# Kernel optimization log

Measured on AMD Instinct MI355X. Metric: run time of the kernel, lower is better.

## Reference

```python
import jax, jax.numpy as jnp
import numpy as np

B, C, H, W = 8, 384, 32, 32
NH = 6
HD = C // NH          # 64
T = H * W             # 1024
EPS = 1e-5            # torch InstanceNorm2d default


def setup_inputs() -> dict:
    key = jax.random.key(0)
    ks = jax.random.split(key, 8)
    s = 1.0 / np.sqrt(C)  # keep pre-softmax logits in a sane range
    x = jax.random.normal(ks[0], (B, C, H, W), dtype=jnp.float32)
    Wq = jax.random.normal(ks[1], (C, C), dtype=jnp.float32) * s
    Wk = jax.random.normal(ks[2], (C, C), dtype=jnp.float32) * s
    Wv = jax.random.normal(ks[3], (C, C), dtype=jnp.float32) * s
    head_w = jax.random.normal(ks[4], (NH, NH), dtype=jnp.float32) * (1.0 / np.sqrt(NH))
    gamma = jnp.ones((NH,), dtype=jnp.float32)
    beta = jnp.zeros((NH,), dtype=jnp.float32)
    projW = jax.random.normal(ks[5], (C, C), dtype=jnp.float32) * s
    projb = jnp.zeros((C,), dtype=jnp.float32)
    return {"x": x, "Wq": Wq, "Wk": Wk, "Wv": Wv, "head_w": head_w,
            "gamma": gamma, "beta": beta, "projW": projW, "projb": projb}


def reference(x, Wq, Wk, Wv, head_w, gamma, beta, projW, projb):
    b, c, h, w = x.shape
    t = h * w
    scale = HD ** (-0.5)
    xf = x.reshape(b, c, t)                               # [B,C,T]
    # 1x1 convs == channel GEMMs; conv weight [Cout,Cin]
    q = jnp.einsum('oc,bct->bot', Wq, xf).reshape(b, NH, HD, t)
    k = jnp.einsum('oc,bct->bot', Wk, xf).reshape(b, NH, HD, t)
    v = jnp.einsum('oc,bct->bot', Wv, xf).reshape(b, NH, HD, t)
    # raw scores [B,h,T,T], scaled
    scores = jnp.einsum('bhdq,bhdt->bhqt', q, k) * scale
    # cross-head 1x1 conv mix: out-head g from in-head h
    mixed = jnp.einsum('gh,bhqt->bgqt', head_w, scores)
    attn = jax.nn.softmax(mixed, axis=-1)
    # InstanceNorm2d over spatial dims (q,T) per (b,head), biased variance
    mean = jnp.mean(attn, axis=(2, 3), keepdims=True)
    var = jnp.var(attn, axis=(2, 3), keepdims=True)
    attn = (attn - mean) * jax.lax.rsqrt(var + EPS)
    attn = attn * gamma[None, :, None, None] + beta[None, :, None, None]
    # value matmul: v is [B,h,d,T]
    out = jnp.einsum('bhqt,bhdt->bhqd', attn, v)          # [B,h,T,d]
    # faithful row-major reshape (matches torch .view(B, T, C))
    out = out.reshape(b, t, c)
    y = out @ projW.T + projb                              # Linear(C,C)
    return jnp.transpose(y, (0, 2, 1)).reshape(b, c, h, w)
```

## Files before the change

kernel.cpp:

```cpp
#include <hip/hip_runtime.h>
#include <hip/hip_bf16.h>
#include <cstdint>

typedef __bf16 bf16_t;
typedef __bf16 bf16x8 __attribute__((ext_vector_type(8)));
typedef float  f32x4  __attribute__((ext_vector_type(4)));

#define MFMA16(a, b, c) __builtin_amdgcn_mfma_f32_16x16x32_bf16((a), (b), (c), 0, 0, 0)

constexpr int BB = 8, CC = 384, NHH = 6, TT = 1024;

union U8 { uint4 u; bf16_t h[8]; };
union U2 { unsigned int u; bf16_t h[2]; };

struct CastArgs {
    const void* src[9];
    bf16_t*     dst[9];
    int         n[9];
};

__global__ __launch_bounds__(256) void cast_kernel(CastArgs a)
{
    const bool isbf = (((const unsigned short*)a.src[5])[0] == 0x3F80u);
    const int ai = blockIdx.y;
    const int n  = a.n[ai];
    bf16_t* dst  = a.dst[ai];
    const int t0     = (blockIdx.x * 256 + threadIdx.x) * 8;
    const int stride = gridDim.x * 256 * 8;
    if (isbf) {
        const bf16_t* s = (const bf16_t*)a.src[ai];
        for (int idx = t0; idx < n; idx += stride) {
            if (idx + 8 <= n) *(uint4*)(dst + idx) = *(const uint4*)(s + idx);
            else for (int j = 0; idx + j < n; ++j) dst[idx + j] = s[idx + j];
        }
    } else {
        const float* s = (const float*)a.src[ai];
        for (int idx = t0; idx < n; idx += stride) {
            if (idx + 8 <= n) {
                f32x4 v0 = *(const f32x4*)(s + idx);
                f32x4 v1 = *(const f32x4*)(s + idx + 4);
                U8 o;
                #pragma unroll
                for (int j = 0; j < 4; ++j) { o.h[j] = (bf16_t)v0[j]; o.h[4 + j] = (bf16_t)v1[j]; }
                *(uint4*)(dst + idx) = o.u;
            } else for (int j = 0; idx + j < n; ++j) dst[idx + j] = (bf16_t)s[idx + j];
        }
    }
}

__global__ __launch_bounds__(256) void qkv_kernel(
    const bf16_t* __restrict__ x,
    const bf16_t* __restrict__ Wq,
    const bf16_t* __restrict__ Wk,
    const bf16_t* __restrict__ Wv,
    bf16_t* __restrict__ qT,
    bf16_t* __restrict__ kT,
    bf16_t* __restrict__ vm)
{
    const int og = blockIdx.x;
    const int tt = blockIdx.y;
    const int b  = blockIdx.z;
    const int t0 = tt * 64;
    const int tid  = threadIdx.x;
    const int lane = tid & 63;
    const int wid  = tid >> 6;
    const int quad = lane >> 4;
    const int l16  = lane & 15;

    __shared__ __align__(16) bf16_t xT[64][CC + 8];

    {
        const bf16_t* xb = x + (size_t)b * CC * TT;
        const int tq = tid & 7;
        const int cp = tid >> 3;
        #pragma unroll
        for (int pass = 0; pass < 6; ++pass) {
            const int c = (pass * 32 + cp) * 2;
            U8 r0, r1;
            r0.u = *(const uint4*)(xb + (size_t)c * TT + t0 + tq * 8);
            r1.u = *(const uint4*)(xb + (size_t)(c + 1) * TT + t0 + tq * 8);
            #pragma unroll
            for (int j = 0; j < 8; ++j) {
                U2 p; p.h[0] = r0.h[j]; p.h[1] = r1.h[j];
                *(unsigned int*)&xT[tq * 8 + j][c] = p.u;
            }
        }
    }
    __syncthreads();

    const bf16_t* W = (og < 2) ? Wq : (og < 4) ? Wk : Wv;
    const int obase = (og & 1) * 192 + wid * 48;

    if (og < 4) {
        f32x4 acc[3][4];
        const f32x4 zero = {0.f, 0.f, 0.f, 0.f};
        #pragma unroll
        for (int mi = 0; mi < 3; ++mi)
            #pragma unroll
            for (int ni = 0; ni < 4; ++ni) acc[mi][ni] = zero;

        for (int k0 = 0; k0 < CC; k0 += 32) {
            bf16x8 afr[3];
            #pragma unroll
            for (int mi = 0; mi < 3; ++mi)
                afr[mi] = *(const bf16x8*)(W + (size_t)(obase + mi * 16 + l16) * CC + k0 + quad * 8);
            #pragma unroll
            for (int ni = 0; ni < 4; ++ni) {
                bf16x8 bfr = *(const bf16x8*)&xT[ni * 16 + l16][k0 + quad * 8];
                #pragma unroll
                for (int mi = 0; mi < 3; ++mi)
                    acc[mi][ni] = MFMA16(afr[mi], bfr, acc[mi][ni]);
            }
        }

        bf16_t* dst = (og < 2) ? qT : kT;
        #pragma unroll
        for (int mi = 0; mi < 3; ++mi)
            #pragma unroll
            for (int ni = 0; ni < 4; ++ni) {
                const int o0 = obase + mi * 16 + quad * 4;
                const int tl = t0 + ni * 16 + l16;
                U2 lo2, hi2;
                lo2.h[0] = (bf16_t)acc[mi][ni][0]; lo2.h[1] = (bf16_t)acc[mi][ni][1];
                hi2.h[0] = (bf16_t)acc[mi][ni][2]; hi2.h[1] = (bf16_t)acc[mi][ni][3];
                uint2 pk; pk.x = lo2.u; pk.y = hi2.u;
                *(uint2*)(dst + ((size_t)b * TT + tl) * CC + o0) = pk;
            }
    } else {
        f32x4 acc[4][3];
        const f32x4 zero = {0.f, 0.f, 0.f, 0.f};
        #pragma unroll
        for (int mi = 0; mi < 4; ++mi)
            #pragma unroll
            for (int ni = 0; ni < 3; ++ni) acc[mi][ni] = zero;

        for (int k0 = 0; k0 < CC; k0 += 32) {
            bf16x8 bfr[3];
            #pragma unroll
            for (int ni = 0; ni < 3; ++ni)
                bfr[ni] = *(const bf16x8*)(W + (size_t)(obase + ni * 16 + l16) * CC + k0 + quad * 8);
            #pragma unroll
            for (int mi = 0; mi < 4; ++mi) {
                bf16x8 afr = *(const bf16x8*)&xT[mi * 16 + l16][k0 + quad * 8];
                #pragma unroll
                for (int ni = 0; ni < 3; ++ni)
                    acc[mi][ni] = MFMA16(afr, bfr[ni], acc[mi][ni]);
            }
        }

        #pragma unroll
        for (int mi = 0; mi < 4; ++mi)
            #pragma unroll
            for (int ni = 0; ni < 3; ++ni) {
                const int ol  = obase + ni * 16 + l16;
                const int tl0 = mi * 16 + quad * 4;
                U2 lo2, hi2;
                lo2.h[0] = (bf16_t)acc[mi][ni][0]; lo2.h[1] = (bf16_t)acc[mi][ni][1];
                hi2.h[0] = (bf16_t)acc[mi][ni][2]; hi2.h[1] = (bf16_t)acc[mi][ni][3];
                uint2 pk; pk.x = lo2.u; pk.y = hi2.u;
                *(uint2*)(vm + ((size_t)b * CC + ol) * TT + t0 + tl0) = pk;
            }
    }
}

__global__ __launch_bounds__(256) void vrow_kernel(const bf16_t* __restrict__ vm,
                                                   float* __restrict__ vrs)
{
    const int bg = blockIdx.x;
    const int d  = threadIdx.x & 63;
    const int qr = threadIdx.x >> 6;
    const bf16_t* row = vm + ((size_t)(bg / 6) * CC + (bg % 6) * 64 + d) * TT + qr * 256;
    float s = 0.f;
    for (int i = 0; i < 256; i += 8) {
        U8 v; v.u = *(const uint4*)(row + i);
        #pragma unroll
        for (int j = 0; j < 8; ++j) s += (float)v.h[j];
    }
    __shared__ float red[4][64];
    red[qr][d] = s;
    __syncthreads();
    if (qr == 0) vrs[bg * 64 + d] = red[0][d] + red[1][d] + red[2][d] + red[3][d];
}

__global__ __launch_bounds__(512, 2) void fused_attn(
    const bf16_t* __restrict__ qT,
    const bf16_t* __restrict__ kT,
    const bf16_t* __restrict__ vm,
    const bf16_t* __restrict__ head_w,
    float* __restrict__ Up,
    float* __restrict__ lp,
    float* __restrict__ l2p)
{
    const int L  = blockIdx.x;
    const int b  = L & 7;
    const int rr = L >> 3;
    const int qt = rr & 15;
    const int th = rr >> 4;

    const int tid = threadIdx.x, lane = tid & 63, wid = tid >> 6;
    const int quad = lane >> 4, l16 = lane & 15;

    __shared__ __align__(16) bf16_t sm[49152];
    bf16_t* Ks = sm;
    bf16_t* Ps = sm + 12288;
    bf16_t* Vs = sm + 24576;
    __shared__ float smix[36];

    if (tid < 36) smix[tid] = 0.125f * (float)head_w[tid];

    const int T0 = th * 512;

    const int tsub = wid & 1;
    const int sqh  = wid >> 1;
    const int pqg  = wid >> 1;
    const int pgg  = wid & 1;

    bf16x8 qf[6][2];
    {
        const bf16_t* Qb = qT + ((size_t)b * TT + qt * 64 + sqh * 16 + l16) * CC + quad * 8;
        #pragma unroll
        for (int kk = 0; kk < 6; ++kk)
            #pragma unroll
            for (int k2 = 0; k2 < 2; ++k2)
                qf[kk][k2] = *(const bf16x8*)(Qb + kk * 64 + k2 * 32);
    }

    const bf16_t* ksrc[3]; const bf16_t* vsrc[3];
    int kdst[3], vdst[3];
    #pragma unroll
    for (int it = 0; it < 3; ++it) {
        const int f  = it * 512 + tid;
        const int kk = f >> 8, krow = (f >> 3) & 31, kch = f & 7;
        ksrc[it] = kT + ((size_t)b * TT + T0 + krow) * CC + kk * 64 + (kch ^ (krow & 7)) * 8;
        kdst[it] = f * 8;
        const int vrow = f >> 2, vch = f & 3;
        vsrc[it] = vm + ((size_t)b * CC + vrow) * TT + T0 + (vch ^ ((vrow >> 1) & 3)) * 8;
        vdst[it] = f * 8;
    }

    uint4 kreg[3], vreg[3];
    #pragma unroll
    for (int it = 0; it < 3; ++it) {
        kreg[it] = *(const uint4*)ksrc[it];
        vreg[it] = *(const uint4*)vsrc[it];
    }
    __syncthreads();

    float mixc[36];
    #pragma unroll
    for (int j = 0; j < 36; ++j)
        mixc[j] = __uint_as_float(__builtin_amdgcn_readfirstlane(__float_as_uint(smix[j])));

    #pragma unroll
    for (int it = 0; it < 3; ++it) {
        *(uint4*)&Ks[kdst[it]] = kreg[it];
        *(uint4*)&Vs[vdst[it]] = vreg[it];
        kreg[it] = *(const uint4*)(ksrc[it] + 32 * CC);
        vreg[it] = *(const uint4*)(vsrc[it] + 32);
    }
    __syncthreads();

    f32x4 Uacc[3][4];
    const f32x4 zero = {0.f, 0.f, 0.f, 0.f};
    #pragma unroll
    for (int hh = 0; hh < 3; ++hh)
        #pragma unroll
        for (int n2 = 0; n2 < 4; ++n2) Uacc[hh][n2] = zero;
    float lacc[6]  = {0.f, 0.f, 0.f, 0.f, 0.f, 0.f};
    float l2acc[6] = {0.f, 0.f, 0.f, 0.f, 0.f, 0.f};

    const int arow  = (tsub * 16 + l16) * 64;
    const int aswz0 = ((quad)     ^ (l16 & 7)) * 8;
    const int aswz1 = ((4 + quad) ^ (l16 & 7)) * 8;
    const int prow  = (sqh * 16 + l16) * 32;
    const int pswzW = ((tsub * 2 + (quad >> 1)) ^ ((l16 >> 1) & 3)) * 8 + (quad & 1) * 4;
    const int parow = (pqg * 16 + l16) * 32;
    const int pswzR = (quad ^ ((l16 >> 1) & 3)) * 8;

    for (int t = 0; t < 16; ++t) {
        f32x4 S[6];
        #pragma unroll
        for (int kk = 0; kk < 6; ++kk) {
            bf16x8 a0 = *(const bf16x8*)&Ks[kk * 2048 + arow + aswz0];
            bf16x8 a1 = *(const bf16x8*)&Ks[kk * 2048 + arow + aswz1];
            S[kk] = MFMA16(a0, qf[kk][0], zero);
            S[kk] = MFMA16(a1, qf[kk][1], S[kk]);
        }
        uint2 pk[6];
        #pragma unroll
        for (int g = 0; g < 6; ++g) {
            float mp[4];
            #pragma unroll
            for (int r = 0; r < 4; ++r) {
                float m = mixc[g * 6] * S[0][r];
                #pragma unroll
                for (int h = 1; h < 6; ++h) m += mixc[g * 6 + h] * S[h][r];
                const float p = __expf(fminf(m, 60.0f));
                lacc[g]  += p;
                l2acc[g] += p * p;
                mp[r] = p;
            }
            U2 lo, hi;
            lo.h[0] = (bf16_t)mp[0]; lo.h[1] = (bf16_t)mp[1];
            hi.h[0] = (bf16_t)mp[2]; hi.h[1] = (bf16_t)mp[3];
            pk[g].x = lo.u; pk[g].y = hi.u;
        }
        __syncthreads();
        #pragma unroll
        for (int it = 0; it < 3; ++it) {
            *(uint4*)&Ks[kdst[it]] = kreg[it];
            *(uint4*)&Vs[((t + 1) & 1) * 12288 + vdst[it]] = vreg[it];
        }
        #pragma unroll
        for (int g = 0; g < 6; ++g)
            *(uint2*)&Ps[g * 2048 + prow + pswzW] = pk[g];
        {
            const int nt = ((t + 2) & 15) * 32;
            #pragma unroll
            for (int it = 0; it < 3; ++it) {
                kreg[it] = *(const uint4*)(ksrc[it] + nt * CC);
                vreg[it] = *(const uint4*)(vsrc[it] + nt);
            }
        }
        __syncthreads();
        const int vb = (t & 1) * 12288;
        #pragma unroll
        for (int hh = 0; hh < 3; ++hh) {
            const int g = pgg * 3 + hh;
            bf16x8 ap = *(const bf16x8*)&Ps[g * 2048 + parow + pswzR];
            #pragma unroll
            for (int n2 = 0; n2 < 4; ++n2) {
                bf16x8 bv = *(const bf16x8*)&Vs[vb + (g * 64 + n2 * 16 + l16) * 32 + pswzR];
                Uacc[hh][n2] = MFMA16(ap, bv, Uacc[hh][n2]);
            }
        }
        __syncthreads();
    }

    float* lredL  = (float*)sm;
    float* l2redL = lredL + 768;
    #pragma unroll
    for (int g = 0; g < 6; ++g) {
        float l = lacc[g], l2 = l2acc[g];
        l  += __shfl_xor(l, 16, 64);  l  += __shfl_xor(l, 32, 64);
        l2 += __shfl_xor(l2, 16, 64); l2 += __shfl_xor(l2, 32, 64);
        if (quad == 0) {
            lredL [wid * 96 + g * 16 + l16] = l;
            l2redL[wid * 96 + g * 16 + l16] = l2;
        }
    }
    __syncthreads();
    if (tid < 384) {
        const int g = tid >> 6, q = tid & 63;
        const int w0 = (q >> 4) * 2, lo = q & 15;
        const float l  = lredL [w0 * 96 + g * 16 + lo] + lredL [(w0 + 1) * 96 + g * 16 + lo];
        const float l2 = l2redL[w0 * 96 + g * 16 + lo] + l2redL[(w0 + 1) * 96 + g * 16 + lo];
        const size_t o = ((size_t)th * 48 + b * 6 + g) * TT + qt * 64 + q;
        lp[o] = l; l2p[o] = l2;
    }

    #pragma unroll
    for (int hh = 0; hh < 3; ++hh) {
        const int g = pgg * 3 + hh;
        float* Ub = Up + ((((size_t)th * 8 + b) * 6 + g) * TT + qt * 64 + pqg * 16) * 64;
        #pragma unroll
        for (int n2 = 0; n2 < 4; ++n2)
            #pragma unroll
            for (int r = 0; r < 4; ++r)
                Ub[(size_t)(quad * 4 + r) * 64 + n2 * 16 + l16] = Uacc[hh][n2][r];
    }
}

__global__ __launch_bounds__(256) void stats_kernel(
    const float* __restrict__ lp, const float* __restrict__ l2p,
    float* __restrict__ linv, float* __restrict__ sq)
{
    const int bg = blockIdx.x, tid = threadIdx.x;
    float c = 0.f;
    for (int q = tid; q < TT; q += 256) {
        const float l  = lp [(size_t)bg * TT + q] + lp [(size_t)(48 + bg) * TT + q];
        const float l2 = l2p[(size_t)bg * TT + q] + l2p[(size_t)(48 + bg) * TT + q];
        const float inv = 1.0f / l;
        linv[bg * TT + q] = inv;
        c += l2 * inv * inv;
    }
    #pragma unroll
    for (int off = 1; off < 64; off <<= 1) c += __shfl_xor(c, off, 64);
    __shared__ float red[4];
    if ((tid & 63) == 0) red[tid >> 6] = c;
    __syncthreads();
    if (tid == 0) sq[bg] = red[0] + red[1] + red[2] + red[3];
}

__global__ __launch_bounds__(256) void proj_kernel(
    const float* __restrict__ Up,
    const float* __restrict__ linv,
    const float* __restrict__ vrs,
    const float* __restrict__ sumsq,
    const bf16_t* __restrict__ gamma,
    const bf16_t* __restrict__ beta,
    const bf16_t* __restrict__ projW,
    const bf16_t* __restrict__ projb,
    float* __restrict__ out)
{
    const int ts = blockIdx.x;
    const int b  = blockIdx.y;
    const int t0 = ts * 32;
    const int tid = threadIdx.x, lane = tid & 63, wid = tid >> 6;
    const int quad = lane >> 4, l16 = lane & 15;

    __shared__ float Ac[6], Cc[6], pb[CC];
    if (tid < 6) {
        const float ss  = sumsq[b * NHH + tid];
        const float var = fmaxf(ss - 1.0f, 0.0f) * (1.0f / 1048576.0f);
        const float a   = (float)gamma[tid] * rsqrtf(var + 1e-5f);
        Ac[tid] = a;
        Cc[tid] = (float)beta[tid] - a * (1.0f / 1024.0f);
    }
    for (int i = tid; i < CC; i += 256) pb[i] = (float)projb[i];
    __syncthreads();

    f32x4 acc[6][2];
    const f32x4 zero = {0.f, 0.f, 0.f, 0.f};
    #pragma unroll
    for (int mi = 0; mi < 6; ++mi)
        #pragma unroll
        for (int ni = 0; ni < 2; ++ni) acc[mi][ni] = zero;

    const float* U0 = Up + (size_t)b * (NHH * TT * 64);
    const float* U1 = Up + (size_t)(8 + b) * (NHH * TT * 64);
    for (int k0 = 0; k0 < CC; k0 += 32) {
        bf16x8 bfr[2];
        #pragma unroll
        for (int ni = 0; ni < 2; ++ni) {
            const int tl = t0 + ni * 16 + l16;
            const int baseoff = tl * CC + k0 + quad * 8;
            const int hh = baseoff >> 16;
            const float li = linv[b * 6144 + (baseoff >> 6)];
            const float A  = Ac[hh];
            const float Cb = Cc[hh];
            f32x4 a0 = *(const f32x4*)(U0 + baseoff);
            f32x4 a1 = *(const f32x4*)(U0 + baseoff + 4);
            f32x4 c0 = *(const f32x4*)(U1 + baseoff);
            f32x4 c1 = *(const f32x4*)(U1 + baseoff + 4);
            U8 z;
            #pragma unroll
            for (int j = 0; j < 8; ++j) {
                const int d = (baseoff + j) & 63;
                const float uv = ((j < 4) ? (a0[j] + c0[j]) : (a1[j - 4] + c1[j - 4])) * li;
                z.h[j] = (bf16_t)(A * uv + Cb * vrs[(b * NHH + hh) * 64 + d]);
            }
            bfr[ni] = *(const bf16x8*)&z;
        }
        #pragma unroll
        for (int mi = 0; mi < 6; ++mi) {
            const int o = wid * 96 + mi * 16 + l16;
            bf16x8 afr = *(const bf16x8*)(projW + (size_t)o * CC + k0 + quad * 8);
            #pragma unroll
            for (int ni = 0; ni < 2; ++ni)
                acc[mi][ni] = MFMA16(afr, bfr[ni], acc[mi][ni]);
        }
    }

    #pragma unroll
    for (int mi = 0; mi < 6; ++mi)
        #pragma unroll
        for (int ni = 0; ni < 2; ++ni)
            #pragma unroll
            for (int r = 0; r < 4; ++r) {
                const int o  = wid * 96 + mi * 16 + quad * 4 + r;
                const int tl = t0 + ni * 16 + l16;
                out[((size_t)b * CC + o) * TT + tl] = acc[mi][ni][r] + pb[o];
            }
}

extern "C" void kernel_launch(void* const* d_in, const int* in_sizes, int n_in,
                              void* d_out, int out_size, void* d_ws, size_t ws_size,
                              hipStream_t stream)
{
    float* outp = (float*)d_out;
    char* ws = (char*)d_ws;

    size_t off = 0;
    auto alloc = [&](size_t bytes) {
        void* p = ws + off;
        off += (bytes + 255) & ~(size_t)255;
        return p;
    };

    const size_t szT = (size_t)BB * TT * CC * sizeof(bf16_t);

    bf16_t* cx  = (bf16_t*)alloc(szT);
    bf16_t* cWq = (bf16_t*)alloc((size_t)CC * CC * 2);
    bf16_t* cWk = (bf16_t*)alloc((size_t)CC * CC * 2);
    bf16_t* cWv = (bf16_t*)alloc((size_t)CC * CC * 2);
    bf16_t* cPW = (bf16_t*)alloc((size_t)CC * CC * 2);
    bf16_t* chw = (bf16_t*)alloc(64 * 2);
    bf16_t* cg  = (bf16_t*)alloc(64 * 2);
    bf16_t* cb  = (bf16_t*)alloc(64 * 2);
    bf16_t* cpb = (bf16_t*)alloc(CC * 2);
    bf16_t* qTb = (bf16_t*)alloc(szT);
    bf16_t* kTb = (bf16_t*)alloc(szT);
    bf16_t* vmb = (bf16_t*)alloc(szT);
    float*  Uh  = (float*)alloc((size_t)2 * BB * NHH * TT * 64 * sizeof(float));
    float*  lpb = (float*)alloc((size_t)2 * 48 * TT * sizeof(float));
    float*  l2b = (float*)alloc((size_t)2 * 48 * TT * sizeof(float));
    float*  lv  = (float*)alloc((size_t)48 * TT * sizeof(float));
    float*  vr  = (float*)alloc(48 * 64 * sizeof(float));
    float*  sq  = (float*)alloc(48 * sizeof(float));

    CastArgs ca;
    bf16_t* dsts[9] = {cx, cWq, cWk, cWv, chw, cg, cb, cPW, cpb};
    for (int i = 0; i < 9; ++i) {
        ca.src[i] = d_in[i];
        ca.dst[i] = dsts[i];
        ca.n[i]   = in_sizes[i];
    }

    cast_kernel<<<dim3(192, 9), 256, 0, stream>>>(ca);
    qkv_kernel<<<dim3(6, 16, 8), 256, 0, stream>>>(cx, cWq, cWk, cWv, qTb, kTb, vmb);
    vrow_kernel<<<48, 256, 0, stream>>>(vmb, vr);
    fused_attn<<<256, 512, 0, stream>>>(qTb, kTb, vmb, chw, Uh, lpb, l2b);
    stats_kernel<<<48, 256, 0, stream>>>(lpb, l2b, lv, sq);
    proj_kernel<<<dim3(32, 8), 256, 0, stream>>>(Uh, lv, vr, sq, cg, cb, cPW, cpb, outp);
}
```

Baseline: 223.7 us.

## Fuse casts into consumers, fold V row sums, restructure attention pipeline

Removes the separate cast kernel, so qkv and proj read fp32 inputs and convert inline. The V row-sum kernel is folded into qkv through atomics. The attention kernel moves to 256-thread blocks with a 4-way key split, async global-to-LDS loads, and in-register P transposition via ds_bpermute instead of an LDS round-trip. This cuts launches and LDS traffic, but doubles the partial-U buffer that proj must read and sum, and adds more partial stats.

New measurement: 343.3 us. 1.53x slower.

```diff
diff --git a/kernel.cpp b/kernel.cpp
--- a/kernel.cpp
+++ b/kernel.cpp
@@ -5,6 +5,7 @@
 typedef __bf16 bf16_t;
 typedef __bf16 bf16x8 __attribute__((ext_vector_type(8)));
 typedef float  f32x4  __attribute__((ext_vector_type(4)));
+typedef int    i32x4  __attribute__((ext_vector_type(4)));
 
 #define MFMA16(a, b, c) __builtin_amdgcn_mfma_f32_16x16x32_bf16((a), (b), (c), 0, 0, 0)
 
@@ -12,50 +13,30 @@
 
 union U8 { uint4 u; bf16_t h[8]; };
 union U2 { unsigned int u; bf16_t h[2]; };
-
-struct CastArgs {
-    const void* src[9];
-    bf16_t*     dst[9];
-    int         n[9];
-};
-
-__global__ __launch_bounds__(256) void cast_kernel(CastArgs a)
-{
-    const bool isbf = (((const unsigned short*)a.src[5])[0] == 0x3F80u);
-    const int ai = blockIdx.y;
-    const int n  = a.n[ai];
-    bf16_t* dst  = a.dst[ai];
-    const int t0     = (blockIdx.x * 256 + threadIdx.x) * 8;
-    const int stride = gridDim.x * 256 * 8;
-    if (isbf) {
-        const bf16_t* s = (const bf16_t*)a.src[ai];
-        for (int idx = t0; idx < n; idx += stride) {
-            if (idx + 8 <= n) *(uint4*)(dst + idx) = *(const uint4*)(s + idx);
-            else for (int j = 0; idx + j < n; ++j) dst[idx + j] = s[idx + j];
-        }
-    } else {
-        const float* s = (const float*)a.src[ai];
-        for (int idx = t0; idx < n; idx += stride) {
-            if (idx + 8 <= n) {
-                f32x4 v0 = *(const f32x4*)(s + idx);
-                f32x4 v1 = *(const f32x4*)(s + idx + 4);
-                U8 o;
-                #pragma unroll
-                for (int j = 0; j < 4; ++j) { o.h[j] = (bf16_t)v0[j]; o.h[4 + j] = (bf16_t)v1[j]; }
-                *(uint4*)(dst + idx) = o.u;
-            } else for (int j = 0; idx + j < n; ++j) dst[idx + j] = (bf16_t)s[idx + j];
-        }
-    }
+union I4B { i32x4 i; bf16x8 v; };
+
+static __device__ __forceinline__ void gload_lds16(const void* g, void* l) {
+    __builtin_amdgcn_global_load_lds((const __attribute__((address_space(1))) void*)g,
+                                     (__attribute__((address_space(3))) void*)l, 16, 0, 0);
+}
+
+static __device__ __forceinline__ bf16x8 cvt8(const float* p) {
+    f32x4 a = *(const f32x4*)p, b = *(const f32x4*)(p + 4);
+    U8 o;
+    #pragma unroll
+    for (int j = 0; j < 4; ++j) { o.h[j] = (bf16_t)a[j]; o.h[4 + j] = (bf16_t)b[j]; }
+    return *(bf16x8*)&o;
 }
 
 __global__ __launch_bounds__(256) void qkv_kernel(
-    const bf16_t* __restrict__ x,
-    const bf16_t* __restrict__ Wq,
-    const bf16_t* __restrict__ Wk,
-    const bf16_t* __restrict__ Wv,
+    const float* __restrict__ x,
+    const float* __restrict__ Wq,
+    const float* __restrict__ Wk,
+    const float* __restrict__ Wv,
     bf16_t* __restrict__ qT,
     bf16_t* __restrict__ kT,
-    bf16_t* __restrict__ vm)
+    bf16_t* __restrict__ vm,
+    float*  __restrict__ vrs)
 {
     const int og = blockIdx.x;
     const int tt = blockIdx.y;
@@ -70,25 +51,28 @@
     __shared__ __align__(16) bf16_t xT[64][CC + 8];
 
     {
-        const bf16_t* xb = x + (size_t)b * CC * TT;
+        const float* xb = x + (size_t)b * CC * TT;
         const int tq = tid & 7;
         const int cp = tid >> 3;
         #pragma unroll
         for (int pass = 0; pass < 6; ++pass) {
             const int c = (pass * 32 + cp) * 2;
-            U8 r0, r1;
-            r0.u = *(const uint4*)(xb + (size_t)c * TT + t0 + tq * 8);
-            r1.u = *(const uint4*)(xb + (size_t)(c + 1) * TT + t0 + tq * 8);
+            const float* r0 = xb + (size_t)c * TT + t0 + tq * 8;
+            const float* r1 = r0 + TT;
+            f32x4 a0 = *(const f32x4*)r0, a1 = *(const f32x4*)(r0 + 4);
+            f32x4 b0 = *(const f32x4*)r1, b1 = *(const f32x4*)(r1 + 4);
             #pragma unroll
             for (int j = 0; j < 8; ++j) {
-                U2 p; p.h[0] = r0.h[j]; p.h[1] = r1.h[j];
+                U2 p;
+                p.h[0] = (bf16_t)((j < 4) ? a0[j] : a1[j - 4]);
+                p.h[1] = (bf16_t)((j < 4) ? b0[j] : b1[j - 4]);
                 *(unsigned int*)&xT[tq * 8 + j][c] = p.u;
             }
         }
     }
     __syncthreads();
 
-    const bf16_t* W = (og < 2) ? Wq : (og < 4) ? Wk : Wv;
+    const float* W = (og < 2) ? Wq : (og < 4) ? Wk : Wv;
     const int obase = (og & 1) * 192 + wid * 48;
 
     if (og < 4) {
@@ -103,7 +87,7 @@
             bf16x8 afr[3];
             #pragma unroll
             for (int mi = 0; mi < 3; ++mi)
-                afr[mi] = *(const bf16x8*)(W + (size_t)(obase + mi * 16 + l16) * CC + k0 + quad * 8);
+                afr[mi] = cvt8(W + (size_t)(obase + mi * 16 + l16) * CC + k0 + quad * 8);
             #pragma unroll
             for (int ni = 0; ni < 4; ++ni) {
                 bf16x8 bfr = *(const bf16x8*)&xT[ni * 16 + l16][k0 + quad * 8];
@@ -138,7 +122,7 @@
             bf16x8 bfr[3];
             #pragma unroll
             for (int ni = 0; ni < 3; ++ni)
-                bfr[ni] = *(const bf16x8*)(W + (size_t)(obase + ni * 16 + l16) * CC + k0 + quad * 8);
+                bfr[ni] = cvt8(W + (size_t)(obase + ni * 16 + l16) * CC + k0 + quad * 8);
             #pragma unroll
             for (int mi = 0; mi < 4; ++mi) {
                 bf16x8 afr = *(const bf16x8*)&xT[mi * 16 + l16][k0 + quad * 8];
@@ -160,33 +144,27 @@
                 uint2 pk; pk.x = lo2.u; pk.y = hi2.u;
                 *(uint2*)(vm + ((size_t)b * CC + ol) * TT + t0 + tl0) = pk;
             }
-    }
-}
-
-__global__ __launch_bounds__(256) void vrow_kernel(const bf16_t* __restrict__ vm,
-                                                   float* __restrict__ vrs)
-{
-    const int bg = blockIdx.x;
-    const int d  = threadIdx.x & 63;
-    const int qr = threadIdx.x >> 6;
-    const bf16_t* row = vm + ((size_t)(bg / 6) * CC + (bg % 6) * 64 + d) * TT + qr * 256;
-    float s = 0.f;
-    for (int i = 0; i < 256; i += 8) {
-        U8 v; v.u = *(const uint4*)(row + i);
-        #pragma unroll
-        for (int j = 0; j < 8; ++j) s += (float)v.h[j];
-    }
-    __shared__ float red[4][64];
-    red[qr][d] = s;
-    __syncthreads();
-    if (qr == 0) vrs[bg * 64 + d] = red[0][d] + red[1][d] + red[2][d] + red[3][d];
-}
-
-__global__ __launch_bounds__(512, 2) void fused_attn(
+
+        #pragma unroll
+        for (int ni = 0; ni < 3; ++ni) {
+            float s = 0.f;
+            #pragma unroll
+            for (int mi = 0; mi < 4; ++mi)
+                #pragma unroll
+                for (int r = 0; r < 4; ++r) s += acc[mi][ni][r];
+            s += __shfl_xor(s, 16, 64);
+            s += __shfl_xor(s, 32, 64);
+            if (quad == 0)
+                atomicAdd(&vrs[b * CC + obase + ni * 16 + l16], s);
+        }
+    }
+}
+
+__global__ __launch_bounds__(256, 2) void fused_attn(
     const bf16_t* __restrict__ qT,
     const bf16_t* __restrict__ kT,
     const bf16_t* __restrict__ vm,
-    const bf16_t* __restrict__ head_w,
+    const float*  __restrict__ head_w,
     float* __restrict__ Up,
     float* __restrict__ lp,
     float* __restrict__ l2p)
@@ -196,178 +174,162 @@
     const int rr = L >> 3;
     const int qt = rr & 15;
     const int th = rr >> 4;
+    const int T0 = th * 256;
 
     const int tid = threadIdx.x, lane = tid & 63, wid = tid >> 6;
     const int quad = lane >> 4, l16 = lane & 15;
 
-    __shared__ __align__(16) bf16_t sm[49152];
+    __shared__ __align__(16) bf16_t sm[36864];
     bf16_t* Ks = sm;
-    bf16_t* Ps = sm + 12288;
-    bf16_t* Vs = sm + 24576;
-    __shared__ float smix[36];
-
-    if (tid < 36) smix[tid] = 0.125f * (float)head_w[tid];
-
-    const int T0 = th * 512;
-
-    const int tsub = wid & 1;
-    const int sqh  = wid >> 1;
-    const int pqg  = wid >> 1;
-    const int pgg  = wid & 1;
-
-    bf16x8 qf[6][2];
-    {
-        const bf16_t* Qb = qT + ((size_t)b * TT + qt * 64 + sqh * 16 + l16) * CC + quad * 8;
-        #pragma unroll
-        for (int kk = 0; kk < 6; ++kk)
-            #pragma unroll
-            for (int k2 = 0; k2 < 2; ++k2)
-                qf[kk][k2] = *(const bf16x8*)(Qb + kk * 64 + k2 * 32);
-    }
-
-    const bf16_t* ksrc[3]; const bf16_t* vsrc[3];
-    int kdst[3], vdst[3];
-    #pragma unroll
-    for (int it = 0; it < 3; ++it) {
-        const int f  = it * 512 + tid;
-        const int kk = f >> 8, krow = (f >> 3) & 31, kch = f & 7;
-        ksrc[it] = kT + ((size_t)b * TT + T0 + krow) * CC + kk * 64 + (kch ^ (krow & 7)) * 8;
-        kdst[it] = f * 8;
-        const int vrow = f >> 2, vch = f & 3;
-        vsrc[it] = vm + ((size_t)b * CC + vrow) * TT + T0 + (vch ^ ((vrow >> 1) & 3)) * 8;
-        vdst[it] = f * 8;
-    }
-
-    uint4 kreg[3], vreg[3];
-    #pragma unroll
-    for (int it = 0; it < 3; ++it) {
-        kreg[it] = *(const uint4*)ksrc[it];
-        vreg[it] = *(const uint4*)vsrc[it];
-    }
-    __syncthreads();
 
     float mixc[36];
     #pragma unroll
-    for (int j = 0; j < 36; ++j)
-        mixc[j] = __uint_as_float(__builtin_amdgcn_readfirstlane(__float_as_uint(smix[j])));
-
-    #pragma unroll
-    for (int it = 0; it < 3; ++it) {
-        *(uint4*)&Ks[kdst[it]] = kreg[it];
-        *(uint4*)&Vs[vdst[it]] = vreg[it];
-        kreg[it] = *(const uint4*)(ksrc[it] + 32 * CC);
-        vreg[it] = *(const uint4*)(vsrc[it] + 32);
-    }
-    __syncthreads();
-
-    f32x4 Uacc[3][4];
+    for (int j = 0; j < 36; ++j) {
+        const float v = 0.125f * head_w[j];
+        mixc[j] = __uint_as_float(__builtin_amdgcn_readfirstlane(__float_as_uint(v)));
+    }
+
+    int koff[6], voff[6], plds[6];
+    #pragma unroll
+    for (int i = 0; i < 6; ++i) {
+        const int p = i * 256 + tid;
+        const int krow = p / 48, pch = p - krow * 48;
+        const int kch = (pch & 56) | ((pch ^ krow) & 7);
+        koff[i] = krow * CC + kch * 8;
+        const int vrow = p >> 2;
+        const int vch  = (p & 3) ^ ((vrow >> 1) & 3);
+        voff[i] = vrow * TT + vch * 8;
+        plds[i] = p * 16;
+    }
+    const bf16_t* kTb = kT + ((size_t)b * TT + T0) * CC;
+    const bf16_t* vmb = vm + (size_t)b * CC * TT + T0;
+    const bf16_t* qp  = qT + ((size_t)b * TT + qt * 64 + wid * 16 + l16) * CC + quad * 8;
+    char* KsB = (char*)sm;
+    char* VsB = (char*)(sm + 12288);
+
+    #pragma unroll
+    for (int i = 0; i < 6; ++i) {
+        gload_lds16(kTb + koff[i], KsB + plds[i]);
+        gload_lds16(vmb + voff[i], VsB + plds[i]);
+    }
+
+    f32x4 U[6][4];
     const f32x4 zero = {0.f, 0.f, 0.f, 0.f};
     #pragma unroll
-    for (int hh = 0; hh < 3; ++hh)
-        #pragma unroll
-        for (int n2 = 0; n2 < 4; ++n2) Uacc[hh][n2] = zero;
+    for (int h = 0; h < 6; ++h)
+        #pragma unroll
+        for (int d = 0; d < 4; ++d) U[h][d] = zero;
     float lacc[6]  = {0.f, 0.f, 0.f, 0.f, 0.f, 0.f};
     float l2acc[6] = {0.f, 0.f, 0.f, 0.f, 0.f, 0.f};
 
-    const int arow  = (tsub * 16 + l16) * 64;
-    const int aswz0 = ((quad)     ^ (l16 & 7)) * 8;
-    const int aswz1 = ((4 + quad) ^ (l16 & 7)) * 8;
-    const int prow  = (sqh * 16 + l16) * 32;
-    const int pswzW = ((tsub * 2 + (quad >> 1)) ^ ((l16 >> 1) & 3)) * 8 + (quad & 1) * 4;
-    const int parow = (pqg * 16 + l16) * 32;
-    const int pswzR = (quad ^ ((l16 >> 1) & 3)) * 8;
-
-    for (int t = 0; t < 16; ++t) {
-        f32x4 S[6];
-        #pragma unroll
-        for (int kk = 0; kk < 6; ++kk) {
-            bf16x8 a0 = *(const bf16x8*)&Ks[kk * 2048 + arow + aswz0];
-            bf16x8 a1 = *(const bf16x8*)&Ks[kk * 2048 + arow + aswz1];
-            S[kk] = MFMA16(a0, qf[kk][0], zero);
-            S[kk] = MFMA16(a1, qf[kk][1], S[kk]);
-        }
-        uint2 pk[6];
+    const int  s3    = l16 & 7;
+    const int  vswz  = (quad ^ ((l16 >> 1) & 3)) * 8 + l16 * 32;
+    const int  addrA = ((quad & 1) * 32 + l16) * 4;
+    const int  addrB = addrA + 64;
+    const bool qlo   = (quad < 2);
+
+    __syncthreads();
+
+    for (int tt = 0; tt < 8; ++tt) {
+        if (tt < 7) {
+            #pragma unroll
+            for (int i = 0; i < 6; ++i)
+                gload_lds16(vmb + (tt + 1) * 32 + voff[i],
+                            VsB + ((tt + 1) & 1) * 24576 + plds[i]);
+        }
+
+        f32x4 S[6][2];
+        bf16x8 qn0 = *(const bf16x8*)(qp);
+        bf16x8 qn1 = *(const bf16x8*)(qp + 32);
+        #pragma unroll
+        for (int h = 0; h < 6; ++h) {
+            bf16x8 q0 = qn0, q1 = qn1;
+            if (h < 5) {
+                qn0 = *(const bf16x8*)(qp + (h + 1) * 64);
+                qn1 = *(const bf16x8*)(qp + (h + 1) * 64 + 32);
+            }
+            #pragma unroll
+            for (int blk = 0; blk < 2; ++blk) {
+                const bf16_t* Ar = Ks + (blk * 16 + l16) * CC + h * 64;
+                bf16x8 a0 = *(const bf16x8*)(Ar + ((quad ^ s3) * 8));
+                bf16x8 a1 = *(const bf16x8*)(Ar + (((4 + quad) ^ s3) * 8));
+                f32x4 s = MFMA16(a0, q0, zero);
+                S[h][blk] = MFMA16(a1, q1, s);
+            }
+        }
+
+        bf16x8 pa[6];
         #pragma unroll
         for (int g = 0; g < 6; ++g) {
-            float mp[4];
-            #pragma unroll
-            for (int r = 0; r < 4; ++r) {
-                float m = mixc[g * 6] * S[0][r];
+            unsigned int uu[2][2];
+            #pragma unroll
+            for (int blk = 0; blk < 2; ++blk) {
+                f32x4 m = mixc[g * 6] * S[0][blk];
                 #pragma unroll
-                for (int h = 1; h < 6; ++h) m += mixc[g * 6 + h] * S[h][r];
-                const float p = __expf(fminf(m, 60.0f));
-                lacc[g]  += p;
-                l2acc[g] += p * p;
-                mp[r] = p;
-            }
-            U2 lo, hi;
-            lo.h[0] = (bf16_t)mp[0]; lo.h[1] = (bf16_t)mp[1];
-            hi.h[0] = (bf16_t)mp[2]; hi.h[1] = (bf16_t)mp[3];
-            pk[g].x = lo.u; pk[g].y = hi.u;
-        }
+                for (int h2 = 1; h2 < 6; ++h2) m += mixc[g * 6 + h2] * S[h2][blk];
+                f32x4 pv;
+                #pragma unroll
+                for (int r = 0; r < 4; ++r) pv[r] = __expf(fminf(m[r], 60.0f));
+                lacc[g]  += pv[0] + pv[1] + pv[2] + pv[3];
+                l2acc[g] += pv[0] * pv[0] + pv[1] * pv[1] + pv[2] * pv[2] + pv[3] * pv[3];
+                U2 lo, hi;
+                lo.h[0] = (bf16_t)pv[0]; lo.h[1] = (bf16_t)pv[1];
+                hi.h[0] = (bf16_t)pv[2]; hi.h[1] = (bf16_t)pv[3];
+                uu[blk][0] = lo.u; uu[blk][1] = hi.u;
+            }
+            int x0 = __builtin_amdgcn_ds_bpermute(addrA, (int)uu[0][0]);
+            int y0 = __builtin_amdgcn_ds_bpermute(addrA, (int)uu[1][0]);
+            int x1 = __builtin_amdgcn_ds_bpermute(addrA, (int)uu[0][1]);
+            int y1 = __builtin_amdgcn_ds_bpermute(addrA, (int)uu[1][1]);
+            int x2 = __builtin_amdgcn_ds_bpermute(addrB, (int)uu[0][0]);
+            int y2 = __builtin_amdgcn_ds_bpermute(addrB, (int)uu[1][0]);
+            int x3 = __builtin_amdgcn_ds_bpermute(addrB, (int)uu[0][1]);
+            int y3 = __builtin_amdgcn_ds_bpermute(addrB, (int)uu[1][1]);
+            I4B c;
+            c.i = (i32x4){qlo ? x0 : y0, qlo ? x1 : y1, qlo ? x2 : y2, qlo ? x3 : y3};
+            pa[g] = c.v;
+        }
+
         __syncthreads();
-        #pragma unroll
-        for (int it = 0; it < 3; ++it) {
-            *(uint4*)&Ks[kdst[it]] = kreg[it];
-            *(uint4*)&Vs[((t + 1) & 1) * 12288 + vdst[it]] = vreg[it];
-        }
-        #pragma unroll
-        for (int g = 0; g < 6; ++g)
-            *(uint2*)&Ps[g * 2048 + prow + pswzW] = pk[g];
-        {
-            const int nt = ((t + 2) & 15) * 32;
-            #pragma unroll
-            for (int it = 0; it < 3; ++it) {
-                kreg[it] = *(const uint4*)(ksrc[it] + nt * CC);
-                vreg[it] = *(const uint4*)(vsrc[it] + nt);
-            }
-        }
+
+        if (tt < 7) {
+            #pragma unroll
+            for (int i = 0; i < 6; ++i)
+                gload_lds16(kTb + (size_t)(tt + 1) * 32 * CC + koff[i], KsB + plds[i]);
+        }
+
+        const bf16_t* Vb = sm + 12288 + (tt & 1) * 12288;
+        #pragma unroll
+        for (int h = 0; h < 6; ++h) {
+            #pragma unroll
+            for (int d = 0; d < 4; ++d) {
+                bf16x8 bv = *(const bf16x8*)(Vb + (h * 64 + d * 16) * 32 + vswz);
+                U[h][d] = MFMA16(pa[h], bv, U[h][d]);
+            }
+        }
+
         __syncthreads();
-        const int vb = (t & 1) * 12288;
-        #pragma unroll
-        for (int hh = 0; hh < 3; ++hh) {
-            const int g = pgg * 3 + hh;
-            bf16x8 ap = *(const bf16x8*)&Ps[g * 2048 + parow + pswzR];
-            #pragma unroll
-            for (int n2 = 0; n2 < 4; ++n2) {
-                bf16x8 bv = *(const bf16x8*)&Vs[vb + (g * 64 + n2 * 16 + l16) * 32 + pswzR];
-                Uacc[hh][n2] = MFMA16(ap, bv, Uacc[hh][n2]);
-            }
-        }
-        __syncthreads();
-    }
-
-    float* lredL  = (float*)sm;
-    float* l2redL = lredL + 768;
+    }
+
     #pragma unroll
     for (int g = 0; g < 6; ++g) {
         float l = lacc[g], l2 = l2acc[g];
         l  += __shfl_xor(l, 16, 64);  l  += __shfl_xor(l, 32, 64);
         l2 += __shfl_xor(l2, 16, 64); l2 += __shfl_xor(l2, 32, 64);
         if (quad == 0) {
-            lredL [wid * 96 + g * 16 + l16] = l;
-            l2redL[wid * 96 + g * 16 + l16] = l2;
-        }
-    }
-    __syncthreads();
-    if (tid < 384) {
-        const int g = tid >> 6, q = tid & 63;
-        const int w0 = (q >> 4) * 2, lo = q & 15;
-        const float l  = lredL [w0 * 96 + g * 16 + lo] + lredL [(w0 + 1) * 96 + g * 16 + lo];
-        const float l2 = l2redL[w0 * 96 + g * 16 + lo] + l2redL[(w0 + 1) * 96 + g * 16 + lo];
-        const size_t o = ((size_t)th * 48 + b * 6 + g) * TT + qt * 64 + q;
-        lp[o] = l; l2p[o] = l2;
-    }
-
-    #pragma unroll
-    for (int hh = 0; hh < 3; ++hh) {
-        const int g = pgg * 3 + hh;
-        float* Ub = Up + ((((size_t)th * 8 + b) * 6 + g) * TT + qt * 64 + pqg * 16) * 64;
-        #pragma unroll
-        for (int n2 = 0; n2 < 4; ++n2)
+            const size_t o = ((size_t)th * 48 + b * 6 + g) * TT + qt * 64 + wid * 16 + l16;
+            lp[o] = l; l2p[o] = l2;
+        }
+    }
+
+    #pragma unroll
+    for (int h = 0; h < 6; ++h) {
+        float* Ub = Up + ((((size_t)th * 8 + b) * 6 + h) * TT + qt * 64 + wid * 16) * 64;
+        #pragma unroll
+        for (int d = 0; d < 4; ++d)
             #pragma unroll
             for (int r = 0; r < 4; ++r)
-                Ub[(size_t)(quad * 4 + r) * 64 + n2 * 16 + l16] = Uacc[hh][n2][r];
+                Ub[(quad * 4 + r) * 64 + d * 16 + l16] = U[h][d][r];
     }
 }
 
@@ -378,8 +340,10 @@
     const int bg = blockIdx.x, tid = threadIdx.x;
     float c = 0.f;
     for (int q = tid; q < TT; q += 256) {
-        const float l  = lp [(size_t)bg * TT + q] + lp [(size_t)(48 + bg) * TT + q];
-        const float l2 = l2p[(size_t)bg * TT + q] + l2p[(size_t)(48 + bg) * TT + q];
+        const float l  = lp [(size_t)bg * TT + q] + lp [(size_t)(48 + bg) * TT + q]
+                       + lp [(size_t)(96 + bg) * TT + q] + lp [(size_t)(144 + bg) * TT + q];
+        const float l2 = l2p[(size_t)bg * TT + q] + l2p[(size_t)(48 + bg) * TT + q]
+                       + l2p[(size_t)(96 + bg) * TT + q] + l2p[(size_t)(144 + bg) * TT + q];
         const float inv = 1.0f / l;
         linv[bg * TT + q] = inv;
         c += l2 * inv * inv;
@@ -397,10 +361,10 @@
     const float* __restrict__ linv,
     const float* __restrict__ vrs,
     const float* __restrict__ sumsq,
-    const bf16_t* __restrict__ gamma,
-    const bf16_t* __restrict__ beta,
-    const bf16_t* __restrict__ projW,
-    const bf16_t* __restrict__ projb,
+    const float* __restrict__ gamma,
+    const float* __restrict__ beta,
+    const float* __restrict__ projW,
+    const float* __restrict__ projb,
     float* __restrict__ out)
 {
     const int ts = blockIdx.x;
@@ -413,11 +377,11 @@
     if (tid < 6) {
         const float ss  = sumsq[b * NHH + tid];
         const float var = fmaxf(ss - 1.0f, 0.0f) * (1.0f / 1048576.0f);
-        const float a   = (float)gamma[tid] * rsqrtf(var + 1e-5f);
+        const float a   = gamma[tid] * rsqrtf(var + 1e-5f);
         Ac[tid] = a;
-        Cc[tid] = (float)beta[tid] - a * (1.0f / 1024.0f);
-    }
-    for (int i = tid; i < CC; i += 256) pb[i] = (float)projb[i];
+        Cc[tid] = beta[tid] - a * (1.0f / 1024.0f);
+    }
+    for (int i = tid; i < CC; i += 256) pb[i] = projb[i];
     __syncthreads();
 
     f32x4 acc[6][2];
@@ -427,8 +391,8 @@
         #pragma unroll
         for (int ni = 0; ni < 2; ++ni) acc[mi][ni] = zero;
 
-    const float* U0 = Up + (size_t)b * (NHH * TT * 64);
-    const float* U1 = Up + (size_t)(8 + b) * (NHH * TT * 64);
+    constexpr size_t PST = (size_t)BB * NHH * TT * 64;
+    const float* Ub = Up + (size_t)b * (NHH * TT * 64);
     for (int k0 = 0; k0 < CC; k0 += 32) {
         bf16x8 bfr[2];
         #pragma unroll
@@ -439,23 +403,25 @@
             const float li = linv[b * 6144 + (baseoff >> 6)];
             const float A  = Ac[hh];
             const float Cb = Cc[hh];
-            f32x4 a0 = *(const f32x4*)(U0 + baseoff);
-            f32x4 a1 = *(const f32x4*)(U0 + baseoff + 4);
-            f32x4 c0 = *(const f32x4*)(U1 + baseoff);
-            f32x4 c1 = *(const f32x4*)(U1 + baseoff + 4);
+            f32x4 s0 = zero, s1 = zero;
+            #pragma unroll
+            for (int p = 0; p < 4; ++p) {
+                s0 += *(const f32x4*)(Ub + p * PST + baseoff);
+                s1 += *(const f32x4*)(Ub + p * PST + baseoff + 4);
+            }
             U8 z;
             #pragma unroll
             for (int j = 0; j < 8; ++j) {
                 const int d = (baseoff + j) & 63;
-                const float uv = ((j < 4) ? (a0[j] + c0[j]) : (a1[j - 4] + c1[j - 4])) * li;
-                z.h[j] = (bf16_t)(A * uv + Cb * vrs[(b * NHH + hh) * 64 + d]);
+                const float uv = ((j < 4) ? s0[j] : s1[j - 4]) * li;
+                z.h[j] = (bf16_t)(A * uv + Cb * vrs[b * CC + hh * 64 + d]);
             }
             bfr[ni] = *(const bf16x8*)&z;
         }
         #pragma unroll
         for (int mi = 0; mi < 6; ++mi) {
             const int o = wid * 96 + mi * 16 + l16;
-            bf16x8 afr = *(const bf16x8*)(projW + (size_t)o * CC + k0 + quad * 8);
+            bf16x8 afr = cvt8(projW + (size_t)o * CC + k0 + quad * 8);
             #pragma unroll
             for (int ni = 0; ni < 2; ++ni)
                 acc[mi][ni] = MFMA16(afr, bfr[ni], acc[mi][ni]);
@@ -490,37 +456,24 @@
 
     const size_t szT = (size_t)BB * TT * CC * sizeof(bf16_t);
 
-    bf16_t* cx  = (bf16_t*)alloc(szT);
-    bf16_t* cWq = (bf16_t*)alloc((size_t)CC * CC * 2);
-    bf16_t* cWk = (bf16_t*)alloc((size_t)CC * CC * 2);
-    bf16_t* cWv = (bf16_t*)alloc((size_t)CC * CC * 2);
-    bf16_t* cPW = (bf16_t*)alloc((size_t)CC * CC * 2);
-    bf16_t* chw = (bf16_t*)alloc(64 * 2);
-    bf16_t* cg  = (bf16_t*)alloc(64 * 2);
-    bf16_t* cb  = (bf16_t*)alloc(64 * 2);
-    bf16_t* cpb = (bf16_t*)alloc(CC * 2);
     bf16_t* qTb = (bf16_t*)alloc(szT);
     bf16_t* kTb = (bf16_t*)alloc(szT);
     bf16_t* vmb = (bf16_t*)alloc(szT);
-    float*  Uh  = (float*)alloc((size_t)2 * BB * NHH * TT * 64 * sizeof(float));
-    float*  lpb = (float*)alloc((size_t)2 * 48 * TT * sizeof(float));
-    float*  l2b = (float*)alloc((size_t)2 * 48 * TT * sizeof(float));
+    float*  Uh  = (float*)alloc((size_t)4 * BB * NHH * TT * 64 * sizeof(float));
+    float*  lpb = (float*)alloc((size_t)4 * 48 * TT * sizeof(float));
+    float*  l2b = (float*)alloc((size_t)4 * 48 * TT * sizeof(float));
     float*  lv  = (float*)alloc((size_t)48 * TT * sizeof(float));
-    float*  vr  = (float*)alloc(48 * 64 * sizeof(float));
+    float*  vr  = (float*)alloc((size_t)BB * CC * sizeof(float));
     float*  sq  = (float*)alloc(48 * sizeof(float));
 
-    CastArgs ca;
-    bf16_t* dsts[9] = {cx, cWq, cWk, cWv, chw, cg, cb, cPW, cpb};
-    for (int i = 0; i < 9; ++i) {
-        ca.src[i] = d_in[i];
-        ca.dst[i] = dsts[i];
-        ca.n[i]   = in_sizes[i];
-    }
-
-    cast_kernel<<<dim3(192, 9), 256, 0, stream>>>(ca);
-    qkv_kernel<<<dim3(6, 16, 8), 256, 0, stream>>>(cx, cWq, cWk, cWv, qTb, kTb, vmb);
-    vrow_kernel<<<48, 256, 0, stream>>>(vmb, vr);
-    fused_attn<<<256, 512, 0, stream>>>(qTb, kTb, vmb, chw, Uh, lpb, l2b);
+    hipMemsetAsync(vr, 0, (size_t)BB * CC * sizeof(float), stream);
+    qkv_kernel<<<dim3(6, 16, 8), 256, 0, stream>>>(
+        (const float*)d_in[0], (const float*)d_in[1], (const float*)d_in[2],
+        (const float*)d_in[3], qTb, kTb, vmb, vr);
+    fused_attn<<<512, 256, 0, stream>>>(
+        qTb, kTb, vmb, (const float*)d_in[4], Uh, lpb, l2b);
     stats_kernel<<<48, 256, 0, stream>>>(lpb, l2b, lv, sq);
-    proj_kernel<<<dim3(32, 8), 256, 0, stream>>>(Uh, lv, vr, sq, cg, cb, cPW, cpb, outp);
-}
+    proj_kernel<<<dim3(32, 8), 256, 0, stream>>>(
+        Uh, lv, vr, sq, (const float*)d_in[5], (const float*)d_in[6],
+        (const float*)d_in[7], (const float*)d_in[8], outp);
+}
```
